# Kernel optimization log

Measured on AMD Instinct MI355X. Metric: run time of the kernel, lower is better.

Reference implementation:

```python
import math
import jax, jax.numpy as jnp
import numpy as np

# hard-coded constants from the source module
SPIRAL_AMP, SPIRAL_PHASE, SPIRAL_SLOPE, SPIRAL_OFFSET = 3.5, 0.0, 0.15, 0.0
MAX_DIGITS, VOCAB_SIZE, POS_DIM, TOK_DIM, QK_DIM = 10, 10, 3, 2, 4

# position map (length 34): source table id and row index within that table
_SRC = np.array([0]*10 + [2] + [0]*10 + [2] + [0]*10 + [1, 2], dtype=np.int32)
_IDX = np.array(list(range(10)) + [0] + list(range(10)) + [1] + list(range(10)) + [0, 2], dtype=np.int32)
# tables are concatenated as [digit(10), z_hi(1), special(3)] -> row offsets per source id
_OFFS = np.array([0, 10, 11], dtype=np.int32)


def _rmsnorm(x, w):
    return x / jnp.sqrt(jnp.mean(x * x, axis=-1, keepdims=True) + 1e-5) * w


def setup_inputs() -> dict:
    key = jax.random.key(0)
    ks = jax.random.split(key, 9)
    B, T = 65536, 34
    idx = jax.random.randint(ks[0], (B, T), 0, VOCAB_SIZE, dtype=jnp.int32)
    return {
        "idx": idx,
        "tok_arc_A": jnp.asarray(2.5, jnp.float32),
        "tok_arc_start": jnp.asarray(-1.2, jnp.float32),
        "tok_arc_stride": jnp.asarray(0.29, jnp.float32),
        "z_hi_pos": 0.1 * jax.random.normal(ks[1], (1, POS_DIM), jnp.float32),
        "special_pos_equals": 0.1 * jax.random.normal(ks[2], (1, POS_DIM), jnp.float32),
        "q_proj_w": 0.5 * jax.random.normal(ks[3], (QK_DIM, POS_DIM), jnp.float32),
        "q_phase_angle": 0.1 * jax.random.normal(ks[4], (1,), jnp.float32),
        "out_proj_A": 0.5 * jax.random.normal(ks[5], (5, 1), jnp.float32),
        "out_proj_B": 0.5 * jax.random.normal(ks[6], (1, 5), jnp.float32),
        "norm_weight": jnp.ones((5,), jnp.float32),
        "fc1_w": 0.5 * jax.random.normal(ks[7], (2, 5), jnp.float32),
        "head_proj_w": 0.5 * jax.random.normal(ks[8], (TOK_DIM, 5), jnp.float32),
    }


def reference(idx, tok_arc_A, tok_arc_start, tok_arc_stride, z_hi_pos,
              special_pos_equals, q_proj_w, q_phase_angle, out_proj_A,
              out_proj_B, norm_weight, fc1_w, head_proj_w):
    B, T = idx.shape
    # token embedding table [V, 2] on an arc
    d = jnp.arange(VOCAB_SIZE, dtype=jnp.float32)
    ang = tok_arc_start + d * tok_arc_stride
    tok_table = tok_arc_A * jnp.stack([jnp.cos(ang), jnp.sin(ang)], axis=1)
    # digit positions on a spiral [10, 3]
    i = jnp.arange(MAX_DIGITS, dtype=jnp.float32)
    a = 2.0 * math.pi * i / MAX_DIGITS + SPIRAL_PHASE
    digit_pos = jnp.stack([SPIRAL_AMP * jnp.cos(a), SPIRAL_AMP * jnp.sin(a),
                           SPIRAL_SLOPE * i + SPIRAL_OFFSET], axis=1)
    special_pos = jnp.concatenate([jnp.zeros((1, POS_DIM)), special_pos_equals,
                                   jnp.zeros((1, POS_DIM))], axis=0)
    full_table = jnp.concatenate([digit_pos, z_hi_pos, special_pos], axis=0)  # [14,3]
    flat = jnp.asarray(_OFFS)[jnp.asarray(_SRC[:T])] + jnp.asarray(_IDX[:T])
    pos = full_table[flat]                                   # [T, 3]

    tok = tok_table[idx]                                     # [B, T, 2]
    x = jnp.concatenate([tok, jnp.broadcast_to(pos[None], (B, T, POS_DIM))], axis=-1)
    h = _rmsnorm(x, norm_weight)
    tok_h, pos_h = h[..., :TOK_DIM], h[..., TOK_DIM:]

    q = pos_h @ q_proj_w.T                                   # [B, T, 4]
    k = q                                                    # identical projection
    v = tok_h @ head_proj_w                                  # [B, T, 5]
    # phase rotation on even/odd pairs of q
    c, s = jnp.cos(q_phase_angle[0]), jnp.sin(q_phase_angle[0])
    q0, q1 = q[..., 0::2], q[..., 1::2]
    q = jnp.stack([q0 * c - q1 * s, q0 * s + q1 * c], axis=-1).reshape(q.shape)

    att = jnp.einsum('btd,bsd->bts', q, k) / math.sqrt(QK_DIM)
    mask = jnp.tril(jnp.ones((T, T), bool))
    att = jax.nn.softmax(jnp.where(mask, att, -jnp.inf), axis=-1)
    out = jnp.einsum('bts,bsh->bth', att, v)                 # [B, T, 5]

    x = x + out @ out_proj_A @ out_proj_B
    ffn = jax.nn.gelu(_rmsnorm(x, norm_weight) @ fc1_w.T, approximate=False)
    x = x + ffn @ head_proj_w
    return (_rmsnorm(x, norm_weight) @ head_proj_w.T) @ tok_table.T  # [B, T, 10]
```

## Files before the change

kernel.cpp:

```cpp
#include <hip/hip_runtime.h>
#include <math.h>

#define T34 34

#define PW_OFF  0
#define TOK_OFF 1156
#define POS_OFF 1184
#define HA_OFF  1320

__global__ __launch_bounds__(64) void prep_kernel(
    const float* __restrict__ pA, const float* __restrict__ pStart,
    const float* __restrict__ pStride, const float* __restrict__ zhi,
    const float* __restrict__ spe, const float* __restrict__ qw,
    const float* __restrict__ qph, const float* __restrict__ opA,
    const float* __restrict__ wn, const float* __restrict__ H,
    float* __restrict__ ws)
{
    __shared__ float sK[T34][4];
    __shared__ float sInv[T34];
    const int t = blockIdx.x;
    const int s = threadIdx.x;
    const float A = pA[0];

    if (s < T34) {
        float p0 = 0.f, p1 = 0.f, p2 = 0.f;
        if (s == 21)      { p0 = spe[0]; p1 = spe[1]; p2 = spe[2]; }
        else if (s == 32) { p0 = zhi[0]; p1 = zhi[1]; p2 = zhi[2]; }
        else if (s != 10 && s != 33) {
            int i = (s < 10) ? s : (s < 21 ? s - 11 : s - 22);
            float a = 0.62831853071795864769f * (float)i;
            p0 = 3.5f * cosf(a); p1 = 3.5f * sinf(a); p2 = 0.15f * (float)i;
        }
        float inv = rsqrtf((A*A + p0*p0 + p1*p1 + p2*p2) * 0.2f + 1e-5f);
        float c0 = p0 * wn[2], c1 = p1 * wn[3], c2 = p2 * wn[4];
        #pragma unroll
        for (int j = 0; j < 4; ++j)
            sK[s][j] = (c0*qw[j*3+0] + c1*qw[j*3+1] + c2*qw[j*3+2]) * inv;
        sInv[s] = inv;
        if (s == t) {
            ws[POS_OFF + 4*t + 0] = p0;
            ws[POS_OFF + 4*t + 1] = p1;
            ws[POS_OFF + 4*t + 2] = p2;
            ws[POS_OFF + 4*t + 3] = 0.f;
        }
    }
    __syncthreads();

    float cc = cosf(qph[0]), sn = sinf(qph[0]);
    float k0 = sK[t][0], k1 = sK[t][1], k2 = sK[t][2], k3 = sK[t][3];
    float q0 = k0*cc - k1*sn, q1 = k0*sn + k1*cc;
    float q2 = k2*cc - k3*sn, q3 = k2*sn + k3*cc;

    float e = 0.f;
    if (s <= t && s < T34) {
        float d = 0.5f*(q0*sK[s][0] + q1*sK[s][1] + q2*sK[s][2] + q3*sK[s][3]);
        e = expf(d);
    }
    float Z = e;
    #pragma unroll
    for (int off = 1; off < 64; off <<= 1) Z += __shfl_xor(Z, off);
    if (s < T34) ws[PW_OFF + t*T34 + s] = (s <= t) ? (e / Z) * sInv[s] : 0.f;

    if (t == 0) {
        if (s < 10) {
            float ang = pStart[0] + (float)s * pStride[0];
            ws[TOK_OFF + 2*s + 0] = A * cosf(ang);
            ws[TOK_OFF + 2*s + 1] = A * sinf(ang);
        } else if (s == 10) {
            float a0 = 0.f, a1 = 0.f;
            #pragma unroll
            for (int h = 0; h < 5; ++h) { a0 += H[h]*opA[h]; a1 += H[5+h]*opA[h]; }
            ws[HA_OFF + 0] = a0 * wn[0];
            ws[HA_OFF + 1] = a1 * wn[1];
        }
    }
}

__global__ __launch_bounds__(448) void micro_kernel(
    const int*  __restrict__ idx,
    const float* __restrict__ pA, const float* __restrict__ pStart,
    const float* __restrict__ pStride,
    const float* __restrict__ opB, const float* __restrict__ wn,
    const float* __restrict__ fc1, const float* __restrict__ H,
    const float* __restrict__ ws,
    float* __restrict__ out)
{
    __shared__ unsigned su[64*35];
    const int lane = threadIdx.x;
    const int b0 = blockIdx.x << 6;

    {
        const float A = pA[0], th0 = pStart[0], dth = pStride[0];
        for (int e = threadIdx.y*64 + lane; e < 64*T34; e += 448) {
            int d = idx[b0*T34 + e];
            unsigned bp = (unsigned)e / 34u;
            int s = e - (int)(bp*34u);
            float ang = th0 + (float)d * dth;
            float ux = A * __cosf(ang);
            float uy = A * __sinf(ang);
            unsigned hx = (__float_as_uint(ux) + 0x8000u) >> 16;
            unsigned hy = (__float_as_uint(uy) + 0x8000u) & 0xffff0000u;
            su[bp*35u + (unsigned)s] = hy | hx;
        }
    }
    __syncthreads();

    int t = blockIdx.y*7 + threadIdx.y;
    if (t >= T34) return;
    const int tu = __builtin_amdgcn_readfirstlane(t);
    const float* __restrict__ Pr = ws + PW_OFF + tu*T34;
    const unsigned* __restrict__ srow = su + lane*35;

    float m2x = 0.f, m2y = 0.f;
    for (int s = 0; s <= tu; ++s) {
        unsigned pk = srow[s];
        float P = Pr[s];
        m2x = fmaf(P, __uint_as_float(pk << 16), m2x);
        m2y = fmaf(P, __uint_as_float(pk & 0xffff0000u), m2y);
    }

    float g = m2x*ws[HA_OFF] + m2y*ws[HA_OFF+1];
    unsigned pkt = srow[tu];
    float x0 = __uint_as_float(pkt << 16)         + g*opB[0];
    float x1 = __uint_as_float(pkt & 0xffff0000u) + g*opB[1];
    float x2 = ws[POS_OFF + 4*tu + 0] + g*opB[2];
    float x3 = ws[POS_OFF + 4*tu + 1] + g*opB[3];
    float x4 = ws[POS_OFF + 4*tu + 2] + g*opB[4];
    float w0 = wn[0], w1 = wn[1], w2 = wn[2], w3 = wn[3], w4 = wn[4];

    float inv1 = rsqrtf((x0*x0 + x1*x1 + x2*x2 + x3*x3 + x4*x4)*0.2f + 1e-5f);
    float h0 = x0*inv1*w0, h1 = x1*inv1*w1, h2 = x2*inv1*w2, h3 = x3*inv1*w3, h4 = x4*inv1*w4;
    float z0 = h0*fc1[0] + h1*fc1[1] + h2*fc1[2] + h3*fc1[3] + h4*fc1[4];
    float z1 = h0*fc1[5] + h1*fc1[6] + h2*fc1[7] + h3*fc1[8] + h4*fc1[9];
    float g0 = 0.5f*z0*(1.f + erff(z0*0.70710678118654752440f));
    float g1 = 0.5f*z1*(1.f + erff(z1*0.70710678118654752440f));
    x0 += g0*H[0] + g1*H[5];
    x1 += g0*H[1] + g1*H[6];
    x2 += g0*H[2] + g1*H[7];
    x3 += g0*H[3] + g1*H[8];
    x4 += g0*H[4] + g1*H[9];
    float inv2 = rsqrtf((x0*x0 + x1*x1 + x2*x2 + x3*x3 + x4*x4)*0.2f + 1e-5f);
    h0 = x0*inv2*w0; h1 = x1*inv2*w1; h2 = x2*inv2*w2; h3 = x3*inv2*w3; h4 = x4*inv2*w4;
    float p0 = h0*H[0] + h1*H[1] + h2*H[2] + h3*H[3] + h4*H[4];
    float p1 = h0*H[5] + h1*H[6] + h2*H[7] + h3*H[8] + h4*H[9];

    const float* tk = ws + TOK_OFF;
    float2* o = (float2*)(out + ((size_t)(b0 + lane)*T34 + (size_t)t)*10u);
    float2 r;
    r.x = p0*tk[0]  + p1*tk[1];  r.y = p0*tk[2]  + p1*tk[3];  o[0] = r;
    r.x = p0*tk[4]  + p1*tk[5];  r.y = p0*tk[6]  + p1*tk[7];  o[1] = r;
    r.x = p0*tk[8]  + p1*tk[9];  r.y = p0*tk[10] + p1*tk[11]; o[2] = r;
    r.x = p0*tk[12] + p1*tk[13]; r.y = p0*tk[14] + p1*tk[15]; o[3] = r;
    r.x = p0*tk[16] + p1*tk[17]; r.y = p0*tk[18] + p1*tk[19]; o[4] = r;
}

extern "C" void kernel_launch(void* const* d_in, const int* in_sizes, int n_in,
                              void* d_out, int out_size, void* d_ws, size_t ws_size,
                              hipStream_t stream)
{
    const int*   idx  = (const int*)  d_in[0];
    const float* pA   = (const float*)d_in[1];
    const float* pSt  = (const float*)d_in[2];
    const float* pSd  = (const float*)d_in[3];
    const float* zhi  = (const float*)d_in[4];
    const float* spe  = (const float*)d_in[5];
    const float* qw   = (const float*)d_in[6];
    const float* qph  = (const float*)d_in[7];
    const float* opA  = (const float*)d_in[8];
    const float* opB  = (const float*)d_in[9];
    const float* wn   = (const float*)d_in[10];
    const float* fc1  = (const float*)d_in[11];
    const float* H    = (const float*)d_in[12];
    float* ws  = (float*)d_ws;
    float* out = (float*)d_out;

    hipLaunchKernelGGL(prep_kernel, dim3(34), dim3(64), 0, stream,
                       pA, pSt, pSd, zhi, spe, qw, qph, opA, wn, H, ws);
    hipLaunchKernelGGL(micro_kernel, dim3(1024, 5), dim3(64, 7), 0, stream,
                       idx, pA, pSt, pSd, opB, wn, fc1, H, ws, out);
}
```

Measured before the change: 161.9 us.

## Process all positions per block and stage outputs in LDS for coalesced stores

The grid's blockIdx.y dimension is removed, so each block handles all 34 positions for its 64 batch rows. This avoids recomputing the token-embedding staging five times. Index loads become int4-vectorized. Results are staged in shared memory and written out as contiguous float2 stores instead of strided per-lane writes. A padded zero row (t=34) is added to the probability and position tables so the 5x7 thread mapping can run unguarded, at the cost of more LDS and more registers per thread.

After: 141.7 us. 1.14x faster.

```diff
diff --git a/kernel.cpp b/kernel.cpp
--- a/kernel.cpp
+++ b/kernel.cpp
@@ -4,9 +4,9 @@
 #define T34 34
 
 #define PW_OFF  0
-#define TOK_OFF 1156
-#define POS_OFF 1184
-#define HA_OFF  1320
+#define TOK_OFF 1190
+#define POS_OFF 1216
+#define HA_OFF  1356
 
 __global__ __launch_bounds__(64) void prep_kernel(
     const float* __restrict__ pA, const float* __restrict__ pStart,
@@ -62,6 +62,7 @@
     if (s < T34) ws[PW_OFF + t*T34 + s] = (s <= t) ? (e / Z) * sInv[s] : 0.f;
 
     if (t == 0) {
+        if (s < T34) ws[PW_OFF + 34*T34 + s] = 0.f;
         if (s < 10) {
             float ang = pStart[0] + (float)s * pStride[0];
             ws[TOK_OFF + 2*s + 0] = A * cosf(ang);
@@ -72,6 +73,11 @@
             for (int h = 0; h < 5; ++h) { a0 += H[h]*opA[h]; a1 += H[5+h]*opA[h]; }
             ws[HA_OFF + 0] = a0 * wn[0];
             ws[HA_OFF + 1] = a1 * wn[1];
+        } else if (s == 11) {
+            ws[POS_OFF + 4*34 + 0] = 0.f;
+            ws[POS_OFF + 4*34 + 1] = 0.f;
+            ws[POS_OFF + 4*34 + 2] = 0.f;
+            ws[POS_OFF + 4*34 + 3] = 0.f;
         }
     }
 }
@@ -86,72 +92,106 @@
     float* __restrict__ out)
 {
     __shared__ unsigned su[64*35];
+    __shared__ float    pr[64*35*2];
+    __shared__ float    stk[20];
     const int lane = threadIdx.x;
-    const int b0 = blockIdx.x << 6;
+    const int ty   = threadIdx.y;
+    const int tid  = ty*64 + lane;
+    const int b0   = blockIdx.x << 6;
 
     {
         const float A = pA[0], th0 = pStart[0], dth = pStride[0];
-        for (int e = threadIdx.y*64 + lane; e < 64*T34; e += 448) {
-            int d = idx[b0*T34 + e];
-            unsigned bp = (unsigned)e / 34u;
-            int s = e - (int)(bp*34u);
-            float ang = th0 + (float)d * dth;
-            float ux = A * __cosf(ang);
-            float uy = A * __sinf(ang);
-            unsigned hx = (__float_as_uint(ux) + 0x8000u) >> 16;
-            unsigned hy = (__float_as_uint(uy) + 0x8000u) & 0xffff0000u;
-            su[bp*35u + (unsigned)s] = hy | hx;
+        if (tid < 20) stk[tid] = ws[TOK_OFF + tid];
+        const int4* src4 = (const int4*)(idx + (size_t)b0*T34);
+        for (int e4 = tid; e4 < (64*T34)/4; e4 += 448) {
+            int4 d4 = src4[e4];
+            int e = e4 << 2;
+            #pragma unroll
+            for (int k = 0; k < 4; ++k) {
+                int d = (k==0) ? d4.x : (k==1) ? d4.y : (k==2) ? d4.z : d4.w;
+                int ee = e + k;
+                unsigned bp = (unsigned)ee / 34u;
+                int s = ee - (int)(bp*34u);
+                float ang = th0 + (float)d*dth;
+                float ux = A*__cosf(ang), uy = A*__sinf(ang);
+                unsigned hx = (__float_as_uint(ux) + 0x8000u) >> 16;
+                unsigned hy = (__float_as_uint(uy) + 0x8000u) & 0xffff0000u;
+                su[bp*35u + (unsigned)s] = hy | hx;
+            }
         }
     }
     __syncthreads();
 
-    int t = blockIdx.y*7 + threadIdx.y;
-    if (t >= T34) return;
-    const int tu = __builtin_amdgcn_readfirstlane(t);
-    const float* __restrict__ Pr = ws + PW_OFF + tu*T34;
-    const unsigned* __restrict__ srow = su + lane*35;
-
-    float m2x = 0.f, m2y = 0.f;
-    for (int s = 0; s <= tu; ++s) {
-        unsigned pk = srow[s];
-        float P = Pr[s];
-        m2x = fmaf(P, __uint_as_float(pk << 16), m2x);
-        m2y = fmaf(P, __uint_as_float(pk & 0xffff0000u), m2y);
-    }
-
-    float g = m2x*ws[HA_OFF] + m2y*ws[HA_OFF+1];
-    unsigned pkt = srow[tu];
-    float x0 = __uint_as_float(pkt << 16)         + g*opB[0];
-    float x1 = __uint_as_float(pkt & 0xffff0000u) + g*opB[1];
-    float x2 = ws[POS_OFF + 4*tu + 0] + g*opB[2];
-    float x3 = ws[POS_OFF + 4*tu + 1] + g*opB[3];
-    float x4 = ws[POS_OFF + 4*tu + 2] + g*opB[4];
-    float w0 = wn[0], w1 = wn[1], w2 = wn[2], w3 = wn[3], w4 = wn[4];
-
-    float inv1 = rsqrtf((x0*x0 + x1*x1 + x2*x2 + x3*x3 + x4*x4)*0.2f + 1e-5f);
-    float h0 = x0*inv1*w0, h1 = x1*inv1*w1, h2 = x2*inv1*w2, h3 = x3*inv1*w3, h4 = x4*inv1*w4;
-    float z0 = h0*fc1[0] + h1*fc1[1] + h2*fc1[2] + h3*fc1[3] + h4*fc1[4];
-    float z1 = h0*fc1[5] + h1*fc1[6] + h2*fc1[7] + h3*fc1[8] + h4*fc1[9];
-    float g0 = 0.5f*z0*(1.f + erff(z0*0.70710678118654752440f));
-    float g1 = 0.5f*z1*(1.f + erff(z1*0.70710678118654752440f));
-    x0 += g0*H[0] + g1*H[5];
-    x1 += g0*H[1] + g1*H[6];
-    x2 += g0*H[2] + g1*H[7];
-    x3 += g0*H[3] + g1*H[8];
-    x4 += g0*H[4] + g1*H[9];
-    float inv2 = rsqrtf((x0*x0 + x1*x1 + x2*x2 + x3*x3 + x4*x4)*0.2f + 1e-5f);
-    h0 = x0*inv2*w0; h1 = x1*inv2*w1; h2 = x2*inv2*w2; h3 = x3*inv2*w3; h4 = x4*inv2*w4;
-    float p0 = h0*H[0] + h1*H[1] + h2*H[2] + h3*H[3] + h4*H[4];
-    float p1 = h0*H[5] + h1*H[6] + h2*H[7] + h3*H[8] + h4*H[9];
-
-    const float* tk = ws + TOK_OFF;
-    float2* o = (float2*)(out + ((size_t)(b0 + lane)*T34 + (size_t)t)*10u);
-    float2 r;
-    r.x = p0*tk[0]  + p1*tk[1];  r.y = p0*tk[2]  + p1*tk[3];  o[0] = r;
-    r.x = p0*tk[4]  + p1*tk[5];  r.y = p0*tk[6]  + p1*tk[7];  o[1] = r;
-    r.x = p0*tk[8]  + p1*tk[9];  r.y = p0*tk[10] + p1*tk[11]; o[2] = r;
-    r.x = p0*tk[12] + p1*tk[13]; r.y = p0*tk[14] + p1*tk[15]; o[3] = r;
-    r.x = p0*tk[16] + p1*tk[17]; r.y = p0*tk[18] + p1*tk[19]; o[4] = r;
+    {
+        const int tyu = __builtin_amdgcn_readfirstlane(ty);
+        const unsigned* __restrict__ srow = su + lane*35;
+        const float* __restrict__ Pb = ws + PW_OFF + tyu*T34;
+
+        float mx[5] = {0,0,0,0,0}, my[5] = {0,0,0,0,0};
+        #pragma unroll
+        for (int s = 0; s < T34; ++s) {
+            unsigned pk = srow[s];
+            float ux = __uint_as_float(pk << 16);
+            float uy = __uint_as_float(pk & 0xffff0000u);
+            #pragma unroll
+            for (int j = 0; j < 5; ++j) {
+                float P = Pb[j*7*T34 + s];
+                mx[j] = fmaf(P, ux, mx[j]);
+                my[j] = fmaf(P, uy, my[j]);
+            }
+        }
+
+        const float hA0 = ws[HA_OFF], hA1 = ws[HA_OFF+1];
+        const float w0=wn[0], w1=wn[1], w2=wn[2], w3=wn[3], w4=wn[4];
+        const float ob0=opB[0], ob1=opB[1], ob2=opB[2], ob3=opB[3], ob4=opB[4];
+
+        #pragma unroll
+        for (int j = 0; j < 5; ++j) {
+            const int t = tyu + 7*j;
+            float g = mx[j]*hA0 + my[j]*hA1;
+            unsigned pkt = srow[t];
+            float x0 = __uint_as_float(pkt << 16)         + g*ob0;
+            float x1 = __uint_as_float(pkt & 0xffff0000u) + g*ob1;
+            float x2 = ws[POS_OFF + 4*t + 0] + g*ob2;
+            float x3 = ws[POS_OFF + 4*t + 1] + g*ob3;
+            float x4 = ws[POS_OFF + 4*t + 2] + g*ob4;
+
+            float inv1 = rsqrtf((x0*x0+x1*x1+x2*x2+x3*x3+x4*x4)*0.2f + 1e-5f);
+            float h0=x0*inv1*w0, h1=x1*inv1*w1, h2=x2*inv1*w2, h3=x3*inv1*w3, h4=x4*inv1*w4;
+            float z0 = h0*fc1[0]+h1*fc1[1]+h2*fc1[2]+h3*fc1[3]+h4*fc1[4];
+            float z1 = h0*fc1[5]+h1*fc1[6]+h2*fc1[7]+h3*fc1[8]+h4*fc1[9];
+            float g0 = 0.5f*z0*(1.f + erff(z0*0.70710678118654752440f));
+            float g1 = 0.5f*z1*(1.f + erff(z1*0.70710678118654752440f));
+            x0 += g0*H[0] + g1*H[5];
+            x1 += g0*H[1] + g1*H[6];
+            x2 += g0*H[2] + g1*H[7];
+            x3 += g0*H[3] + g1*H[8];
+            x4 += g0*H[4] + g1*H[9];
+            float inv2 = rsqrtf((x0*x0+x1*x1+x2*x2+x3*x3+x4*x4)*0.2f + 1e-5f);
+            h0=x0*inv2*w0; h1=x1*inv2*w1; h2=x2*inv2*w2; h3=x3*inv2*w3; h4=x4*inv2*w4;
+            float p0 = h0*H[0]+h1*H[1]+h2*H[2]+h3*H[3]+h4*H[4];
+            float p1 = h0*H[5]+h1*H[6]+h2*H[7]+h3*H[8]+h4*H[9];
+            pr[(lane*35 + t)*2 + 0] = p0;
+            pr[(lane*35 + t)*2 + 1] = p1;
+        }
+    }
+    __syncthreads();
+
+    {
+        float2* __restrict__ o = (float2*)out + (size_t)b0*170;
+        for (int e = tid; e < 64*170; e += 448) {
+            int bp = e / 170;
+            int r  = e - 170*bp;
+            int t  = r / 5;
+            int j2 = r - 5*t;
+            float p0 = pr[(bp*35 + t)*2 + 0];
+            float p1 = pr[(bp*35 + t)*2 + 1];
+            float2 v;
+            v.x = p0*stk[4*j2+0] + p1*stk[4*j2+1];
+            v.y = p0*stk[4*j2+2] + p1*stk[4*j2+3];
+            o[e] = v;
+        }
+    }
 }
 
 extern "C" void kernel_launch(void* const* d_in, const int* in_sizes, int n_in,
@@ -176,6 +216,6 @@
 
     hipLaunchKernelGGL(prep_kernel, dim3(34), dim3(64), 0, stream,
                        pA, pSt, pSd, zhi, spe, qw, qph, opA, wn, H, ws);
-    hipLaunchKernelGGL(micro_kernel, dim3(1024, 5), dim3(64, 7), 0, stream,
+    hipLaunchKernelGGL(micro_kernel, dim3(1024), dim3(64, 7), 0, stream,
                        idx, pA, pSt, pSd, opB, wn, fc1, H, ws, out);
 }
```
